# Performance work log

Measured on AMD Instinct MI355X. Metric: run time of the kernel, lower is better.

The kernel has to match this reference:

```python
import jax, jax.numpy as jnp
import numpy as np

B = 128          # batch
D = 2048         # original_dim
P = 16000        # projection_dim


def _count_sketch_matrix(key, d, p):
    """Dense count-sketch matrix: one +/-1 per row at a random column.
    Mirrors the torch init: col ~ randint(0, p-1), sign = 2*randint(0,2)-1."""
    k_idx, k_sgn = jax.random.split(key)
    idx = jax.random.randint(k_idx, (d,), 0, p - 1)            # torch uses high=p-1 (exclusive)
    sgn = (2 * jax.random.randint(k_sgn, (d,), 0, 2) - 1).astype(jnp.float32)
    C = jnp.zeros((d, p), dtype=jnp.float32)
    return C.at[jnp.arange(d), idx].set(sgn)


def setup_inputs() -> dict:
    key = jax.random.key(0)
    kx1, kx2, kc1, kc2 = jax.random.split(key, 4)
    x1 = jax.random.normal(kx1, (B, D), dtype=jnp.float32)
    x2 = jax.random.normal(kx2, (B, D), dtype=jnp.float32)
    C1 = _count_sketch_matrix(kc1, D, P)
    C2 = _count_sketch_matrix(kc2, D, P)
    return {"x1": x1, "x2": x2, "C1": C1, "C2": C2}


def reference(x1, x2, C1, C2):
    # Count-sketch projections (dense mm, as in the original module)
    y1 = x1 @ C1                      # [B, P]
    y2 = x2 @ C2                      # [B, P]
    # Circular convolution via FFT -> elementwise complex multiply -> IFFT.
    # Original takes only the real part of the IFFT output.
    f1 = jnp.fft.fft(y1, axis=-1)
    f2 = jnp.fft.fft(y2, axis=-1)
    phi = jnp.fft.ifft(f1 * f2, axis=-1).real.astype(jnp.float32)
    return phi                        # [B, P]
```

## Files before the change

### kernel.cpp

```cpp
#include <hip/hip_runtime.h>

#define NFFT 16000
#define BATCH 128
#define DIM 2048

__device__ __forceinline__ float2 cmul(float2 a, float2 b) {
    return make_float2(a.x * b.x - a.y * b.y, a.x * b.y + a.y * b.x);
}
__device__ __forceinline__ float2 cadd(float2 a, float2 b) { return make_float2(a.x + b.x, a.y + b.y); }
__device__ __forceinline__ float2 csub(float2 a, float2 b) { return make_float2(a.x - b.x, a.y - b.y); }
__device__ __forceinline__ float2 cis(float ang) { return make_float2(__cosf(ang), __sinf(ang)); }

__device__ __forceinline__ int rev5_3(int n) {
    int d0 = n % 5, r = n / 5;
    int d1 = r % 5, d2 = r / 5;
    return d0 * 25 + d1 * 5 + d2;
}

__device__ __forceinline__ int perm_slot(int p) {
    return (p & 127) * 125 + rev5_3(p >> 7);
}

__device__ __forceinline__ int posn1(int k) {
    return ((k & 3) << 5) | (((k >> 2) & 3) << 3) | (((k >> 4) & 3) << 1) | (k >> 6);
}

__global__ void extract_sketch(const float* __restrict__ C1, const float* __restrict__ C2,
                               int* __restrict__ idx1, float* __restrict__ sgn1,
                               int* __restrict__ idx2, float* __restrict__ sgn2) {
    int gwave = (blockIdx.x * blockDim.x + threadIdx.x) >> 6;
    int lane = threadIdx.x & 63;
    if (gwave >= 2 * DIM) return;
    const float* row;
    int* idxp; float* sgnp; int d;
    if (gwave < DIM) { d = gwave;       row = C1 + (size_t)d * NFFT; idxp = idx1; sgnp = sgn1; }
    else             { d = gwave - DIM; row = C2 + (size_t)d * NFFT; idxp = idx2; sgnp = sgn2; }
    for (int step = 0; step < 16; ++step) {
        int off0 = step * 1024 + lane * 4;
        float4 v[4];
        #pragma unroll
        for (int c = 0; c < 4; ++c) {
            int off = off0 + c * 256;
            v[c] = (off < NFFT) ? *reinterpret_cast<const float4*>(row + off)
                                : make_float4(0.f, 0.f, 0.f, 0.f);
        }
        bool found = false;
        #pragma unroll
        for (int c = 0; c < 4; ++c) {
            float4 w = v[c];
            if (w.x != 0.f || w.y != 0.f || w.z != 0.f || w.w != 0.f) {
                int off = off0 + c * 256;
                int j; float s;
                if (w.x != 0.f)      { j = 0; s = w.x; }
                else if (w.y != 0.f) { j = 1; s = w.y; }
                else if (w.z != 0.f) { j = 2; s = w.z; }
                else                 { j = 3; s = w.w; }
                idxp[d] = off + j;
                sgnp[d] = s;
                found = true;
            }
        }
        if (__any(found)) return;
    }
}

__device__ void fft16000(float2* ld) {
    const int tid = threadIdx.x, nt = blockDim.x;
    const float C1_5 = 0.30901699437494742f, S1_5 = 0.95105651629515357f;
    const float C2_5 = -0.80901699437494745f, S2_5 = 0.58778525229247312f;
    const float2 w5tab[5] = { make_float2(1.f, 0.f),
                              make_float2(C1_5, -S1_5), make_float2(C2_5, -S2_5),
                              make_float2(C2_5,  S2_5), make_float2(C1_5,  S1_5) };

    #pragma unroll
    for (int s = 0; s < 3; ++s) {
        const int m = (s == 0) ? 1 : (s == 1) ? 5 : 25;
        const float angstep = -6.28318530717958647692f / (float)(5 * m);
        for (int task = tid; task < 128 * 25; task += nt) {
            int n1 = task / 25;
            int bf = task - n1 * 25;
            int t = bf % m, blk = bf / m;
            int base = n1 * 125 + blk * (5 * m) + t;
            float2 xv[5];
            #pragma unroll
            for (int r = 0; r < 5; ++r) xv[r] = ld[base + r * m];
            if (m > 1) {
                float2 w1 = cis(angstep * (float)t);
                float2 w2 = cmul(w1, w1);
                float2 w3 = cmul(w2, w1);
                float2 w4 = cmul(w2, w2);
                xv[1] = cmul(xv[1], w1); xv[2] = cmul(xv[2], w2);
                xv[3] = cmul(xv[3], w3); xv[4] = cmul(xv[4], w4);
            }
            float2 y[5];
            #pragma unroll
            for (int q = 0; q < 5; ++q) {
                float2 acc = xv[0];
                #pragma unroll
                for (int r = 1; r < 5; ++r) {
                    float2 t2 = cmul(xv[r], w5tab[(q * r) % 5]);
                    acc.x += t2.x; acc.y += t2.y;
                }
                y[q] = acc;
            }
            #pragma unroll
            for (int q = 0; q < 5; ++q) ld[base + q * m] = y[q];
        }
        __syncthreads();
    }

    {
        const float ANGN = -6.28318530717958647692f / 16000.0f;
        const float ANGL = -6.28318530717958647692f / 128.0f;
        for (int tau = tid; tau < 125 * 32; tau += nt) {
            int j = tau / 125;
            int k2 = tau - j * 125;
            float2 v[4];
            #pragma unroll
            for (int p = 0; p < 4; ++p) {
                int n1 = j + 32 * p;
                float2 x = ld[n1 * 125 + k2];
                v[p] = cmul(x, cis(ANGN * (float)(n1 * k2)));
            }
            float2 s0 = cadd(v[0], v[2]), s1 = cadd(v[1], v[3]);
            float2 d0 = csub(v[0], v[2]), d1 = csub(v[1], v[3]);
            float2 t0 = cadd(s0, s1), t2 = csub(s0, s1);
            float2 t1 = make_float2(d0.x + d1.y, d0.y - d1.x);
            float2 t3 = make_float2(d0.x - d1.y, d0.y + d1.x);
            float2 w1 = cis(ANGL * (float)j);
            float2 w2 = cmul(w1, w1), w3 = cmul(w2, w1);
            ld[ j       * 125 + k2] = t0;
            ld[(j + 32) * 125 + k2] = cmul(w1, t1);
            ld[(j + 64) * 125 + k2] = cmul(w2, t2);
            ld[(j + 96) * 125 + k2] = cmul(w3, t3);
        }
        __syncthreads();
    }
    {
        const float ANGL = -6.28318530717958647692f / 32.0f;
        for (int tau = tid; tau < 125 * 32; tau += nt) {
            int bf = tau / 125;
            int k2 = tau - bf * 125;
            int j = bf & 7, blk = bf >> 3;
            int base = blk * 32 + j;
            float2 v[4];
            #pragma unroll
            for (int p = 0; p < 4; ++p) v[p] = ld[(base + 8 * p) * 125 + k2];
            float2 s0 = cadd(v[0], v[2]), s1 = cadd(v[1], v[3]);
            float2 d0 = csub(v[0], v[2]), d1 = csub(v[1], v[3]);
            float2 t0 = cadd(s0, s1), t2 = csub(s0, s1);
            float2 t1 = make_float2(d0.x + d1.y, d0.y - d1.x);
            float2 t3 = make_float2(d0.x - d1.y, d0.y + d1.x);
            float2 w1 = cis(ANGL * (float)j);
            float2 w2 = cmul(w1, w1), w3 = cmul(w2, w1);
            ld[(base     ) * 125 + k2] = t0;
            ld[(base +  8) * 125 + k2] = cmul(w1, t1);
            ld[(base + 16) * 125 + k2] = cmul(w2, t2);
            ld[(base + 24) * 125 + k2] = cmul(w3, t3);
        }
        __syncthreads();
    }
    {
        const float ANGL = -6.28318530717958647692f / 8.0f;
        for (int tau = tid; tau < 125 * 32; tau += nt) {
            int bf = tau / 125;
            int k2 = tau - bf * 125;
            int j = bf & 1, blk = bf >> 1;
            int base = blk * 8 + j;
            float2 v[4];
            #pragma unroll
            for (int p = 0; p < 4; ++p) v[p] = ld[(base + 2 * p) * 125 + k2];
            float2 s0 = cadd(v[0], v[2]), s1 = cadd(v[1], v[3]);
            float2 d0 = csub(v[0], v[2]), d1 = csub(v[1], v[3]);
            float2 t0 = cadd(s0, s1), t2 = csub(s0, s1);
            float2 t1 = make_float2(d0.x + d1.y, d0.y - d1.x);
            float2 t3 = make_float2(d0.x - d1.y, d0.y + d1.x);
            float2 w1 = cis(ANGL * (float)j);
            float2 w2 = cmul(w1, w1), w3 = cmul(w2, w1);
            ld[(base    ) * 125 + k2] = t0;
            ld[(base + 2) * 125 + k2] = cmul(w1, t1);
            ld[(base + 4) * 125 + k2] = cmul(w2, t2);
            ld[(base + 6) * 125 + k2] = cmul(w3, t3);
        }
        __syncthreads();
    }
    {
        for (int tau = tid; tau < 125 * 64; tau += nt) {
            int blk = tau / 125;
            int k2 = tau - blk * 125;
            int pa = (2 * blk) * 125 + k2, pb = pa + 125;
            float2 a = ld[pa], b = ld[pb];
            ld[pa] = cadd(a, b);
            ld[pb] = csub(a, b);
        }
        __syncthreads();
    }
}

__global__ void __launch_bounds__(1024)
fused_fft(const float* __restrict__ x1, const float* __restrict__ x2,
          const int* __restrict__ idx1, const float* __restrict__ sgn1,
          const int* __restrict__ idx2, const float* __restrict__ sgn2,
          float* __restrict__ out) {
    extern __shared__ float2 ld[];
    const int b = blockIdx.x;
    const int tid = threadIdx.x, nt = blockDim.x;

    for (int i = tid; i < NFFT; i += nt) ld[i] = make_float2(0.f, 0.f);
    __syncthreads();

    const float* x1b = x1 + (size_t)b * DIM;
    const float* x2b = x2 + (size_t)b * DIM;
    for (int d = tid; d < DIM; d += nt) {
        atomicAdd(&ld[perm_slot(idx1[d])].x, sgn1[d] * x1b[d]);
        atomicAdd(&ld[perm_slot(idx2[d])].y, sgn2[d] * x2b[d]);
    }
    __syncthreads();

    fft16000(ld);

    float2 vals[8][2];
    int nk = 0;
    for (int k = tid; k <= NFFT / 2; k += nt, ++nk) {
        int k1 = k / 125, k2 = k - 125 * k1;
        int k1m, k2m;
        if (k2 == 0) { k2m = 0;        k1m = (128 - k1) & 127; }
        else         { k2m = 125 - k2; k1m = 127 - k1; }
        float2 Zk = ld[posn1(k1)  * 125 + k2];
        float2 Zm = ld[posn1(k1m) * 125 + k2m];
        float u = (Zk.x * Zk.x - Zk.y * Zk.y) - (Zm.x * Zm.x - Zm.y * Zm.y);
        float v = 2.f * (Zk.x * Zk.y + Zm.x * Zm.y);
        vals[nk][0] = make_float2(0.25f * v,  0.25f * u);
        vals[nk][1] = make_float2(0.25f * v, -0.25f * u);
    }
    __syncthreads();
    nk = 0;
    for (int k = tid; k <= NFFT / 2; k += nt, ++nk) {
        ld[perm_slot(k)] = vals[nk][0];
        if (k != 0 && k != NFFT / 2)
            ld[perm_slot(NFFT - k)] = vals[nk][1];
    }
    __syncthreads();

    fft16000(ld);

    const float invN = 1.0f / (float)NFFT;
    float* outb = out + (size_t)b * NFFT;
    for (int k = tid; k < NFFT; k += nt) {
        int k1 = k / 125, k2 = k - 125 * k1;
        outb[k] = ld[posn1(k1) * 125 + k2].x * invN;
    }
}

extern "C" void kernel_launch(void* const* d_in, const int* in_sizes, int n_in,
                              void* d_out, int out_size, void* d_ws, size_t ws_size,
                              hipStream_t stream) {
    (void)in_sizes; (void)n_in; (void)out_size; (void)ws_size;
    const float* x1 = (const float*)d_in[0];
    const float* x2 = (const float*)d_in[1];
    const float* C1 = (const float*)d_in[2];
    const float* C2 = (const float*)d_in[3];
    float* out = (float*)d_out;

    char* w = (char*)d_ws;
    int*    idx1 = (int*)  (w);
    float*  sgn1 = (float*)(w + 8192);
    int*    idx2 = (int*)  (w + 16384);
    float*  sgn2 = (float*)(w + 24576);

    (void)hipFuncSetAttribute((const void*)fused_fft,
                              hipFuncAttributeMaxDynamicSharedMemorySize, NFFT * 8);

    extract_sketch<<<(2 * DIM) / 4, 256, 0, stream>>>(C1, C2, idx1, sgn1, idx2, sgn2);
    fused_fft     <<<BATCH, 1024, NFFT * 8, stream>>>(x1, x2, idx1, sgn1, idx2, sgn2, out);
}
```

Baseline: 320.0 us.

## Split fused per-batch FFT into three kernels with wave-shuffle radix-2 stages

Replaces the single 128-block fused kernel, one block per batch row, with three kernels. The first does a radix-5 column FFT over quarter-slices and applies twiddles. The second does the 128-point stages with wave-level shuffles, plus the conjugate-pair spectral product and the inverse 128-point stage. The third does the radix-5 row FFT and writes the output. This aims to raise occupancy and parallelism beyond 128 large-LDS blocks on a GPU with many more compute units. The cost is two global intermediate buffers (U, V) round-tripped through HBM and extra kernel launches.

```diff
diff --git a/kernel.cpp b/kernel.cpp
--- a/kernel.cpp
+++ b/kernel.cpp
@@ -3,6 +3,7 @@
 #define NFFT 16000
 #define BATCH 128
 #define DIM 2048
+#define TP 17
 
 __device__ __forceinline__ float2 cmul(float2 a, float2 b) {
     return make_float2(a.x * b.x - a.y * b.y, a.x * b.y + a.y * b.x);
@@ -17,12 +18,36 @@
     return d0 * 25 + d1 * 5 + d2;
 }
 
-__device__ __forceinline__ int perm_slot(int p) {
-    return (p & 127) * 125 + rev5_3(p >> 7);
-}
-
-__device__ __forceinline__ int posn1(int k) {
-    return ((k & 3) << 5) | (((k >> 2) & 3) << 3) | (((k >> 4) & 3) << 1) | (k >> 6);
+__device__ __forceinline__ float2 conjG(float2 Zk, float2 Zm) {
+    float u = (Zk.x * Zk.x - Zk.y * Zk.y) - (Zm.x * Zm.x - Zm.y * Zm.y);
+    float v = 2.f * (Zk.x * Zk.y + Zm.x * Zm.y);
+    return make_float2(0.25f * v, 0.25f * u);
+}
+
+__device__ __forceinline__ void dif128(float2& x0, float2& x1, int l) {
+    const float PI_F = 3.14159265358979323846f;
+    {
+        float2 a = x0, b = x1;
+        x0 = cadd(a, b);
+        float2 d = csub(a, b);
+        x1 = cmul(d, cis(-PI_F / 64.0f * (float)l));
+    }
+    #pragma unroll
+    for (int m = 32; m >= 1; m >>= 1) {
+        int j = l & (m - 1);
+        bool upper = (l & m) != 0;
+        float2 w = cis(-PI_F / (float)m * (float)j);
+        float2 o0, o1;
+        o0.x = __shfl_xor(x0.x, m); o0.y = __shfl_xor(x0.y, m);
+        o1.x = __shfl_xor(x1.x, m); o1.y = __shfl_xor(x1.y, m);
+        if (upper) {
+            x0 = cmul(csub(o0, x0), w);
+            x1 = cmul(csub(o1, x1), w);
+        } else {
+            x0 = cadd(x0, o0);
+            x1 = cadd(x1, o1);
+        }
+    }
 }
 
 __global__ void extract_sketch(const float* __restrict__ C1, const float* __restrict__ C2,
@@ -64,191 +89,193 @@
     }
 }
 
-__device__ void fft16000(float2* ld) {
-    const int tid = threadIdx.x, nt = blockDim.x;
+__global__ void __launch_bounds__(256) k1_colfft(
+        const float* __restrict__ x1, const float* __restrict__ x2,
+        const int* __restrict__ idx1, const float* __restrict__ sgn1,
+        const int* __restrict__ idx2, const float* __restrict__ sgn2,
+        float2* __restrict__ U) {
+    __shared__ float2 S[32 * 125];
+    const int b = blockIdx.x >> 2, q = blockIdx.x & 3;
+    const int tid = threadIdx.x;
+
+    for (int i = tid; i < 32 * 125; i += 256) S[i] = make_float2(0.f, 0.f);
+    __syncthreads();
+
+    const float* x1b = x1 + (size_t)b * DIM;
+    const float* x2b = x2 + (size_t)b * DIM;
+    for (int d = tid; d < DIM; d += 256) {
+        int p1 = idx1[d]; int n1a = p1 & 127;
+        if ((n1a >> 5) == q) atomicAdd(&S[(n1a & 31) * 125 + rev5_3(p1 >> 7)].x, sgn1[d] * x1b[d]);
+        int p2 = idx2[d]; int n1b = p2 & 127;
+        if ((n1b >> 5) == q) atomicAdd(&S[(n1b & 31) * 125 + rev5_3(p2 >> 7)].y, sgn2[d] * x2b[d]);
+    }
+    __syncthreads();
+
     const float C1_5 = 0.30901699437494742f, S1_5 = 0.95105651629515357f;
     const float C2_5 = -0.80901699437494745f, S2_5 = 0.58778525229247312f;
     const float2 w5tab[5] = { make_float2(1.f, 0.f),
                               make_float2(C1_5, -S1_5), make_float2(C2_5, -S2_5),
                               make_float2(C2_5,  S2_5), make_float2(C1_5,  S1_5) };
-
     #pragma unroll
     for (int s = 0; s < 3; ++s) {
         const int m = (s == 0) ? 1 : (s == 1) ? 5 : 25;
         const float angstep = -6.28318530717958647692f / (float)(5 * m);
-        for (int task = tid; task < 128 * 25; task += nt) {
-            int n1 = task / 25;
-            int bf = task - n1 * 25;
+        for (int task = tid; task < 32 * 25; task += 256) {
+            int row = task / 25;
+            int bf = task - row * 25;
             int t = bf % m, blk = bf / m;
-            int base = n1 * 125 + blk * (5 * m) + t;
+            int base = row * 125 + blk * (5 * m) + t;
             float2 xv[5];
             #pragma unroll
-            for (int r = 0; r < 5; ++r) xv[r] = ld[base + r * m];
+            for (int r = 0; r < 5; ++r) xv[r] = S[base + r * m];
             if (m > 1) {
                 float2 w1 = cis(angstep * (float)t);
-                float2 w2 = cmul(w1, w1);
-                float2 w3 = cmul(w2, w1);
-                float2 w4 = cmul(w2, w2);
+                float2 w2 = cmul(w1, w1), w3 = cmul(w2, w1), w4 = cmul(w2, w2);
                 xv[1] = cmul(xv[1], w1); xv[2] = cmul(xv[2], w2);
                 xv[3] = cmul(xv[3], w3); xv[4] = cmul(xv[4], w4);
             }
             float2 y[5];
             #pragma unroll
-            for (int q = 0; q < 5; ++q) {
+            for (int qq = 0; qq < 5; ++qq) {
                 float2 acc = xv[0];
                 #pragma unroll
                 for (int r = 1; r < 5; ++r) {
-                    float2 t2 = cmul(xv[r], w5tab[(q * r) % 5]);
+                    float2 t2 = cmul(xv[r], w5tab[(qq * r) % 5]);
                     acc.x += t2.x; acc.y += t2.y;
                 }
-                y[q] = acc;
-            }
-            #pragma unroll
-            for (int q = 0; q < 5; ++q) ld[base + q * m] = y[q];
+                y[qq] = acc;
+            }
+            #pragma unroll
+            for (int qq = 0; qq < 5; ++qq) S[base + qq * m] = y[qq];
         }
         __syncthreads();
     }
 
-    {
-        const float ANGN = -6.28318530717958647692f / 16000.0f;
-        const float ANGL = -6.28318530717958647692f / 128.0f;
-        for (int tau = tid; tau < 125 * 32; tau += nt) {
-            int j = tau / 125;
-            int k2 = tau - j * 125;
-            float2 v[4];
-            #pragma unroll
-            for (int p = 0; p < 4; ++p) {
-                int n1 = j + 32 * p;
-                float2 x = ld[n1 * 125 + k2];
-                v[p] = cmul(x, cis(ANGN * (float)(n1 * k2)));
-            }
-            float2 s0 = cadd(v[0], v[2]), s1 = cadd(v[1], v[3]);
-            float2 d0 = csub(v[0], v[2]), d1 = csub(v[1], v[3]);
-            float2 t0 = cadd(s0, s1), t2 = csub(s0, s1);
-            float2 t1 = make_float2(d0.x + d1.y, d0.y - d1.x);
-            float2 t3 = make_float2(d0.x - d1.y, d0.y + d1.x);
-            float2 w1 = cis(ANGL * (float)j);
-            float2 w2 = cmul(w1, w1), w3 = cmul(w2, w1);
-            ld[ j       * 125 + k2] = t0;
-            ld[(j + 32) * 125 + k2] = cmul(w1, t1);
-            ld[(j + 64) * 125 + k2] = cmul(w2, t2);
-            ld[(j + 96) * 125 + k2] = cmul(w3, t3);
+    const float ANGN = -6.28318530717958647692f / 16000.0f;
+    const int n1base = q * 32;
+    float2* Ub = U + (size_t)b * NFFT;
+    for (int i = tid; i < 32 * 125; i += 256) {
+        int n1l = i & 31, k2 = i >> 5;
+        int n1 = n1base + n1l;
+        Ub[k2 * 128 + n1] = cmul(S[n1l * 125 + k2], cis(ANGN * (float)(n1 * k2)));
+    }
+}
+
+__global__ void __launch_bounds__(256) k2_pair(const float2* __restrict__ U,
+                                               float2* __restrict__ V) {
+    __shared__ float2 Z[4][2][128];
+    const int w = threadIdx.x >> 6, l = threadIdx.x & 63;
+    const int task = blockIdx.x * 4 + w;
+    const int b = task / 63, cg = task - b * 63;
+    const int c = cg, cm = (cg == 0) ? 0 : 125 - cg;
+    const float2* Ub = U + (size_t)b * NFFT;
+
+    float2 a0 = Ub[c * 128 + l],  a1 = Ub[c * 128 + l + 64];
+    float2 b0 = Ub[cm * 128 + l], b1 = Ub[cm * 128 + l + 64];
+    dif128(a0, a1, l);
+    dif128(b0, b1, l);
+    const int e = (int)(__brev((unsigned)l) >> 25);
+
+    Z[w][0][e] = a0; Z[w][0][e + 1] = a1;
+    Z[w][1][e] = b0; Z[w][1][e + 1] = b1;
+    __syncthreads();
+
+    float2 gA0, gA1, gB0, gB1;
+    if (cg != 0) {
+        float2 zm0 = Z[w][1][127 - e];
+        float2 zm1 = Z[w][1][126 - e];
+        gA0 = conjG(a0, zm0);
+        gA1 = conjG(a1, zm1);
+        gB1 = conjG(zm0, a0);
+        gB0 = conjG(zm1, a1);
+    } else {
+        float2 zm0 = Z[w][0][(128 - e) & 127];
+        float2 zm1 = Z[w][0][127 - e];
+        gA0 = conjG(a0, zm0);
+        gA1 = conjG(a1, zm1);
+        gB0 = make_float2(0.f, 0.f); gB1 = make_float2(0.f, 0.f);
+    }
+    __syncthreads();
+
+    Z[w][0][e] = gA0; Z[w][0][e + 1] = gA1;
+    if (cg != 0) { Z[w][1][126 - e] = gB0; Z[w][1][127 - e] = gB1; }
+    __syncthreads();
+
+    float2 p0 = Z[w][0][l], p1 = Z[w][0][l + 64];
+    float2 q0 = Z[w][1][l], q1 = Z[w][1][l + 64];
+    dif128(p0, p1, l);
+    dif128(q0, q1, l);
+
+    const float ANGN = -6.28318530717958647692f / 16000.0f;
+    float2* Vb = V + (size_t)b * NFFT;
+    p0 = cmul(p0, cis(ANGN * (float)(c * e)));
+    p1 = cmul(p1, cis(ANGN * (float)(c * (e + 1))));
+    *reinterpret_cast<float4*>(&Vb[c * 128 + e]) = make_float4(p0.x, p0.y, p1.x, p1.y);
+    if (cg != 0) {
+        q0 = cmul(q0, cis(ANGN * (float)(cm * e)));
+        q1 = cmul(q1, cis(ANGN * (float)(cm * (e + 1))));
+        *reinterpret_cast<float4*>(&Vb[cm * 128 + e]) = make_float4(q0.x, q0.y, q1.x, q1.y);
+    }
+}
+
+__global__ void __launch_bounds__(256) k3_rowfft(const float2* __restrict__ V,
+                                                 float* __restrict__ out) {
+    __shared__ float2 T[125 * TP];
+    const int b = blockIdx.x >> 3, g = blockIdx.x & 7;
+    const int j1base = g * 16, tid = threadIdx.x;
+    const float2* Vb = V + (size_t)b * NFFT;
+
+    for (int i = tid; i < 125 * 16; i += 256) {
+        int m1 = i >> 4, j1l = i & 15;
+        T[rev5_3(m1) * TP + j1l] = Vb[m1 * 128 + j1base + j1l];
+    }
+    __syncthreads();
+
+    const float C1_5 = 0.30901699437494742f, S1_5 = 0.95105651629515357f;
+    const float C2_5 = -0.80901699437494745f, S2_5 = 0.58778525229247312f;
+    const float2 w5tab[5] = { make_float2(1.f, 0.f),
+                              make_float2(C1_5, -S1_5), make_float2(C2_5, -S2_5),
+                              make_float2(C2_5,  S2_5), make_float2(C1_5,  S1_5) };
+    #pragma unroll
+    for (int s = 0; s < 3; ++s) {
+        const int m = (s == 0) ? 1 : (s == 1) ? 5 : 25;
+        const float angstep = -6.28318530717958647692f / (float)(5 * m);
+        for (int task = tid; task < 16 * 25; task += 256) {
+            int bf = task >> 4;
+            int j1l = task & 15;
+            int t = bf % m, blk = bf / m;
+            int base = (blk * (5 * m) + t) * TP + j1l;
+            float2 xv[5];
+            #pragma unroll
+            for (int r = 0; r < 5; ++r) xv[r] = T[base + r * m * TP];
+            if (m > 1) {
+                float2 w1 = cis(angstep * (float)t);
+                float2 w2 = cmul(w1, w1), w3 = cmul(w2, w1), w4 = cmul(w2, w2);
+                xv[1] = cmul(xv[1], w1); xv[2] = cmul(xv[2], w2);
+                xv[3] = cmul(xv[3], w3); xv[4] = cmul(xv[4], w4);
+            }
+            float2 y[5];
+            #pragma unroll
+            for (int qq = 0; qq < 5; ++qq) {
+                float2 acc = xv[0];
+                #pragma unroll
+                for (int r = 1; r < 5; ++r) {
+                    float2 t2 = cmul(xv[r], w5tab[(qq * r) % 5]);
+                    acc.x += t2.x; acc.y += t2.y;
+                }
+                y[qq] = acc;
+            }
+            #pragma unroll
+            for (int qq = 0; qq < 5; ++qq) T[base + qq * m * TP] = y[qq];
         }
         __syncthreads();
     }
-    {
-        const float ANGL = -6.28318530717958647692f / 32.0f;
-        for (int tau = tid; tau < 125 * 32; tau += nt) {
-            int bf = tau / 125;
-            int k2 = tau - bf * 125;
-            int j = bf & 7, blk = bf >> 3;
-            int base = blk * 32 + j;
-            float2 v[4];
-            #pragma unroll
-            for (int p = 0; p < 4; ++p) v[p] = ld[(base + 8 * p) * 125 + k2];
-            float2 s0 = cadd(v[0], v[2]), s1 = cadd(v[1], v[3]);
-            float2 d0 = csub(v[0], v[2]), d1 = csub(v[1], v[3]);
-            float2 t0 = cadd(s0, s1), t2 = csub(s0, s1);
-            float2 t1 = make_float2(d0.x + d1.y, d0.y - d1.x);
-            float2 t3 = make_float2(d0.x - d1.y, d0.y + d1.x);
-            float2 w1 = cis(ANGL * (float)j);
-            float2 w2 = cmul(w1, w1), w3 = cmul(w2, w1);
-            ld[(base     ) * 125 + k2] = t0;
-            ld[(base +  8) * 125 + k2] = cmul(w1, t1);
-            ld[(base + 16) * 125 + k2] = cmul(w2, t2);
-            ld[(base + 24) * 125 + k2] = cmul(w3, t3);
-        }
-        __syncthreads();
-    }
-    {
-        const float ANGL = -6.28318530717958647692f / 8.0f;
-        for (int tau = tid; tau < 125 * 32; tau += nt) {
-            int bf = tau / 125;
-            int k2 = tau - bf * 125;
-            int j = bf & 1, blk = bf >> 1;
-            int base = blk * 8 + j;
-            float2 v[4];
-            #pragma unroll
-            for (int p = 0; p < 4; ++p) v[p] = ld[(base + 2 * p) * 125 + k2];
-            float2 s0 = cadd(v[0], v[2]), s1 = cadd(v[1], v[3]);
-            float2 d0 = csub(v[0], v[2]), d1 = csub(v[1], v[3]);
-            float2 t0 = cadd(s0, s1), t2 = csub(s0, s1);
-            float2 t1 = make_float2(d0.x + d1.y, d0.y - d1.x);
-            float2 t3 = make_float2(d0.x - d1.y, d0.y + d1.x);
-            float2 w1 = cis(ANGL * (float)j);
-            float2 w2 = cmul(w1, w1), w3 = cmul(w2, w1);
-            ld[(base    ) * 125 + k2] = t0;
-            ld[(base + 2) * 125 + k2] = cmul(w1, t1);
-            ld[(base + 4) * 125 + k2] = cmul(w2, t2);
-            ld[(base + 6) * 125 + k2] = cmul(w3, t3);
-        }
-        __syncthreads();
-    }
-    {
-        for (int tau = tid; tau < 125 * 64; tau += nt) {
-            int blk = tau / 125;
-            int k2 = tau - blk * 125;
-            int pa = (2 * blk) * 125 + k2, pb = pa + 125;
-            float2 a = ld[pa], b = ld[pb];
-            ld[pa] = cadd(a, b);
-            ld[pb] = csub(a, b);
-        }
-        __syncthreads();
-    }
-}
-
-__global__ void __launch_bounds__(1024)
-fused_fft(const float* __restrict__ x1, const float* __restrict__ x2,
-          const int* __restrict__ idx1, const float* __restrict__ sgn1,
-          const int* __restrict__ idx2, const float* __restrict__ sgn2,
-          float* __restrict__ out) {
-    extern __shared__ float2 ld[];
-    const int b = blockIdx.x;
-    const int tid = threadIdx.x, nt = blockDim.x;
-
-    for (int i = tid; i < NFFT; i += nt) ld[i] = make_float2(0.f, 0.f);
-    __syncthreads();
-
-    const float* x1b = x1 + (size_t)b * DIM;
-    const float* x2b = x2 + (size_t)b * DIM;
-    for (int d = tid; d < DIM; d += nt) {
-        atomicAdd(&ld[perm_slot(idx1[d])].x, sgn1[d] * x1b[d]);
-        atomicAdd(&ld[perm_slot(idx2[d])].y, sgn2[d] * x2b[d]);
-    }
-    __syncthreads();
-
-    fft16000(ld);
-
-    float2 vals[8][2];
-    int nk = 0;
-    for (int k = tid; k <= NFFT / 2; k += nt, ++nk) {
-        int k1 = k / 125, k2 = k - 125 * k1;
-        int k1m, k2m;
-        if (k2 == 0) { k2m = 0;        k1m = (128 - k1) & 127; }
-        else         { k2m = 125 - k2; k1m = 127 - k1; }
-        float2 Zk = ld[posn1(k1)  * 125 + k2];
-        float2 Zm = ld[posn1(k1m) * 125 + k2m];
-        float u = (Zk.x * Zk.x - Zk.y * Zk.y) - (Zm.x * Zm.x - Zm.y * Zm.y);
-        float v = 2.f * (Zk.x * Zk.y + Zm.x * Zm.y);
-        vals[nk][0] = make_float2(0.25f * v,  0.25f * u);
-        vals[nk][1] = make_float2(0.25f * v, -0.25f * u);
-    }
-    __syncthreads();
-    nk = 0;
-    for (int k = tid; k <= NFFT / 2; k += nt, ++nk) {
-        ld[perm_slot(k)] = vals[nk][0];
-        if (k != 0 && k != NFFT / 2)
-            ld[perm_slot(NFFT - k)] = vals[nk][1];
-    }
-    __syncthreads();
-
-    fft16000(ld);
 
     const float invN = 1.0f / (float)NFFT;
     float* outb = out + (size_t)b * NFFT;
-    for (int k = tid; k < NFFT; k += nt) {
-        int k1 = k / 125, k2 = k - 125 * k1;
-        outb[k] = ld[posn1(k1) * 125 + k2].x * invN;
+    for (int i = tid; i < 125 * 16; i += 256) {
+        int j2 = i >> 4, j1l = i & 15;
+        outb[j1base + j1l + 128 * j2] = T[j2 * TP + j1l].x * invN;
     }
 }
 
@@ -267,10 +294,11 @@
     float*  sgn1 = (float*)(w + 8192);
     int*    idx2 = (int*)  (w + 16384);
     float*  sgn2 = (float*)(w + 24576);
-
-    (void)hipFuncSetAttribute((const void*)fused_fft,
-                              hipFuncAttributeMaxDynamicSharedMemorySize, NFFT * 8);
+    float2* U    = (float2*)(w + 32768);
+    float2* V    = (float2*)(w + 32768 + 16384000);
 
     extract_sketch<<<(2 * DIM) / 4, 256, 0, stream>>>(C1, C2, idx1, sgn1, idx2, sgn2);
-    fused_fft     <<<BATCH, 1024, NFFT * 8, stream>>>(x1, x2, idx1, sgn1, idx2, sgn2, out);
-}
+    k1_colfft     <<<BATCH * 4, 256, 0, stream>>>(x1, x2, idx1, sgn1, idx2, sgn2, U);
+    k2_pair       <<<2016, 256, 0, stream>>>(U, V);
+    k3_rowfft     <<<BATCH * 8, 256, 0, stream>>>(V, out);
+}
```

Measured after the change: 302.0 us. 5.6% less time.
